# Performance work log

Hardware: AMD Instinct MI355X
Metric: run time of the kernel (lower is better)

The kernel has to match this reference:

```python
import jax, jax.numpy as jnp
import numpy as np

INIT_W = 0.1  # init_weight uniform range


def setup_inputs() -> dict:
    key = jax.random.key(0)
    kq, kk, kwq, kwk, ka = jax.random.split(key, 5)
    B, b, t_q, t_k = 2, 16, 64, 128
    qs = ks = nu = 512
    query = jax.random.normal(kq, (B, b, t_q, qs), dtype=jnp.float32)
    keys = jax.random.normal(kk, (B, b, t_k, ks), dtype=jnp.float32)
    # torch Linear weight layout: (out_features, in_features), per fusion slice
    Wq = (jax.random.uniform(kwq, (B, nu, qs), dtype=jnp.float32) * 2 - 1) * INIT_W
    Wk = (jax.random.uniform(kwk, (B, nu, ks), dtype=jnp.float32) * 2 - 1) * INIT_W
    linear_att = (jax.random.uniform(ka, (nu,), dtype=jnp.float32) * 2 - 1) * INIT_W
    return {"query": query, "keys": keys, "Wq": Wq, "Wk": Wk, "linear_att": linear_att}


def reference(query, keys, Wq, Wk, linear_att):
    # query: (B, b, t_q, query_size), keys: (B, b, t_k, key_size)
    # HFTA-fused linear projections (no bias): y = x @ W.T per fusion slice
    pq = jnp.einsum('Bbqi,Boi->Bbqo', query, Wq)   # (B, b, t_q, n)
    pk = jnp.einsum('Bbki,Boi->Bbko', keys, Wk)    # (B, b, t_k, n)
    # Bahdanau additive score: tanh(q + k) . v  (broadcast add over t_q x t_k)
    sum_qk = pq[:, :, :, None, :] + pk[:, :, None, :, :]   # (B, b, t_q, t_k, n)
    scores = jnp.einsum('Bbqkn,n->Bbqk', jnp.tanh(sum_qk), linear_att)
    scores_normalized = jax.nn.softmax(scores, axis=-1)    # (B, b, t_q, t_k)
    # context uses RAW keys (not projected)
    context = jnp.einsum('Bbqk,Bbkn->Bbqn', scores_normalized, keys)
    return context, scores_normalized
```

## Files before the change

### kernel.cpp

```cpp
#include <hip/hip_runtime.h>


#define DEV_INLINE __device__ __forceinline__

constexpr float C2    = 2.8853900817779268f;
constexpr float LOG2E = 1.4426950408889634f;

typedef _Float16 f16x8 __attribute__((ext_vector_type(8)));
typedef float    f32x16 __attribute__((ext_vector_type(16)));

DEV_INLINE unsigned int pk2(float a, float b) {
    auto h = __builtin_amdgcn_cvt_pkrtz(a, b);
    return __builtin_bit_cast(unsigned int, h);
}

DEV_INLINE float rcp_nr(float d) {
    float y = __builtin_bit_cast(float, 0x7EF311C3u - __builtin_bit_cast(unsigned int, d));
    y = y * (2.0f - d * y);
    y = y * (2.0f - d * y);
    return y;
}

#define GL2LDS16(g, l) __builtin_amdgcn_global_load_lds( \
    (const __attribute__((address_space(1))) void*)(g),  \
    (__attribute__((address_space(3))) void*)(l), 16, 0, 0)

__global__ __launch_bounds__(256)
void cvt_f16_kernel(const float* __restrict__ query, const float* __restrict__ keys,
                    const float* __restrict__ Wq,    const float* __restrict__ Wk,
                    uint2* __restrict__ dst)
{
    const int i4 = blockIdx.x * 256 + threadIdx.x;
    const float* src; int base;
    if (i4 < 262144)      { src = query; base = 0; }
    else if (i4 < 786432) { src = keys;  base = 262144; }
    else if (i4 < 917504) { src = Wq;    base = 786432; }
    else                  { src = Wk;    base = 917504; }
    const float4 v = *reinterpret_cast<const float4*>(src + (size_t)(i4 - base) * 4);
    dst[i4] = make_uint2(pk2(v.x, v.y), pk2(v.z, v.w));
}

__global__ __launch_bounds__(256)
void proj_mfma_kernel(const _Float16* __restrict__ X16,
                      float* __restrict__ pqT, float* __restrict__ pkT)
{
    __shared__ __align__(16) unsigned char smem[24576];

    const int bid = (blockIdx.x & 7) * 48 + (blockIdx.x >> 3);

    int Bi, mt, tt, tkshift;
    const _Float16 *Wb, *Xb; float* Y;
    if (bid < 128) {
        Bi = bid >> 6; mt = (bid >> 4) & 3; tt = bid & 15;
        Xb = X16 + ((size_t)Bi * 1024 + tt * 64) * 512;
        Wb = X16 + 3145728 + (size_t)Bi * 262144 + (size_t)(mt * 128) * 512;
        Y = pqT; tkshift = 6;
    } else {
        const int b2 = bid - 128;
        Bi = b2 >> 7; mt = (b2 >> 5) & 3; tt = b2 & 31;
        Xb = X16 + 1048576 + ((size_t)Bi * 2048 + tt * 64) * 512;
        Wb = X16 + 3670016 + (size_t)Bi * 262144 + (size_t)(mt * 128) * 512;
        Y = pkT; tkshift = 7;
    }
    const int tid = threadIdx.x;

    auto srcoff = [](int u) {
        const int row = u >> 2, s = (u & 3) ^ ((row >> 1) & 3);
        return (size_t)row * 512 + s * 8;
    };
    const _Float16* gA0 = Wb + srcoff(tid);
    const _Float16* gA1 = Wb + srcoff(tid + 256);
    const _Float16* gB  = Xb + srcoff(tid);
    unsigned char* const ldsA0 = smem + tid * 16;
    unsigned char* const ldsA1 = smem + 4096 + tid * 16;
    unsigned char* const ldsB  = smem + 8192 + tid * 16;

    const int wid = tid >> 6, lane = tid & 63;
    const int wm = wid >> 1, wn = wid & 1;
    const int r31 = lane & 31, h = lane >> 5;
    auto lofs = [](int row, int slot) {
        return row * 64 + ((slot ^ ((row >> 1) & 3)) * 16);
    };
    const int rowA0 = wm * 64 + r31, rowA1 = rowA0 + 32, rowB = wn * 32 + r31;
    const int a00 = lofs(rowA0, h),     a01 = lofs(rowA0, 2 + h);
    const int a10 = lofs(rowA1, h),     a11 = lofs(rowA1, 2 + h);
    const int b0  = 8192 + lofs(rowB, h), b1 = 8192 + lofs(rowB, 2 + h);

    f32x16 acc0, acc1;
#pragma unroll
    for (int i = 0; i < 16; ++i) { acc0[i] = 0.f; acc1[i] = 0.f; }

    GL2LDS16(gA0, ldsA0);
    GL2LDS16(gA1, ldsA1);
    GL2LDS16(gB,  ldsB);
    asm volatile("s_waitcnt vmcnt(0)" ::: "memory");
    __builtin_amdgcn_s_barrier();

    for (int ks = 0; ks < 16; ++ks) {
        const int buf = ks & 1;
        if (ks < 15) {
            const int ko = (ks + 1) * 32, bo = (buf ^ 1) * 12288;
            GL2LDS16(gA0 + ko, ldsA0 + bo);
            GL2LDS16(gA1 + ko, ldsA1 + bo);
            GL2LDS16(gB  + ko, ldsB  + bo);
        }
        const unsigned char* sb = smem + buf * 12288;
        const f16x8 fa00 = *reinterpret_cast<const f16x8*>(sb + a00);
        const f16x8 fa01 = *reinterpret_cast<const f16x8*>(sb + a01);
        const f16x8 fa10 = *reinterpret_cast<const f16x8*>(sb + a10);
        const f16x8 fa11 = *reinterpret_cast<const f16x8*>(sb + a11);
        const f16x8 fb0  = *reinterpret_cast<const f16x8*>(sb + b0);
        const f16x8 fb1  = *reinterpret_cast<const f16x8*>(sb + b1);
        acc0 = __builtin_amdgcn_mfma_f32_32x32x16_f16(fa00, fb0, acc0, 0, 0, 0);
        acc0 = __builtin_amdgcn_mfma_f32_32x32x16_f16(fa01, fb1, acc0, 0, 0, 0);
        acc1 = __builtin_amdgcn_mfma_f32_32x32x16_f16(fa10, fb0, acc1, 0, 0, 0);
        acc1 = __builtin_amdgcn_mfma_f32_32x32x16_f16(fa11, fb1, acc1, 0, 0, 0);
        if (ks < 15) {
            asm volatile("s_waitcnt vmcnt(0)" ::: "memory");
            __builtin_amdgcn_s_barrier();
        }
    }

    const int TK = 1 << tkshift;
    const int trow = tt * 64 + wn * 32 + r31;
    const int slice = Bi * 16 + (trow >> tkshift);
    const int t = trow & (TK - 1);
    const int nf0 = mt * 128 + wm * 64 + 4 * h;
#pragma unroll
    for (int ab = 0; ab < 2; ++ab) {
        const f32x16 acc = ab ? acc1 : acc0;
#pragma unroll
        for (int reg = 0; reg < 16; ++reg) {
            const int nf = nf0 + ab * 32 + (reg & 3) + 8 * (reg >> 2);
            Y[((size_t)(slice * 512 + nf) << tkshift) + t] = acc[reg] * C2;
        }
    }
}

DEV_INLINE float wave_rmax(float v) {
#pragma unroll
    for (int off = 32; off; off >>= 1) v = fmaxf(v, __shfl_xor(v, off, 64));
    return v;
}
DEV_INLINE float wave_rsum(float v) {
#pragma unroll
    for (int off = 32; off; off >>= 1) v += __shfl_xor(v, off, 64);
    return v;
}

__global__ __launch_bounds__(1024)
void score_ctx_kernel(const float* __restrict__ pqT,
                      const float* __restrict__ pkT,
                      const float* __restrict__ vatt,
                      const float* __restrict__ keys,
                      float* __restrict__ sc_out,
                      float* __restrict__ ctx)
{
    const int xcd = blockIdx.x & 7, ix = blockIdx.x >> 3;
    const int slice = xcd * 4 + (ix >> 4);
    const int q0    = (ix & 15) * 4;
    const int tid   = threadIdx.x;
    const int k     = tid & 127;
    const int nh    = tid >> 7;

    __shared__ __align__(16) float pql[512][4];
    __shared__ float wl[512];
    __shared__ float partial[7][4][128];
    __shared__ __align__(16) float sc[128][4];
    __shared__ __align__(16) float4 ctxp[4][4][128];
    __shared__ float wredm[8], wreds[8], wsum[8];

    if (tid < 512) {
        const float vv = vatt[tid];
        wl[tid] = -2.f * vv;
        const float4 q4 = *reinterpret_cast<const float4*>(
            pqT + ((size_t)slice * 512 + tid) * 64 + q0);
        *reinterpret_cast<float4*>(&pql[tid][0]) = q4;
        const float s = wave_rsum(vv);
        if ((tid & 63) == 0) wsum[tid >> 6] = s;
    }
    __syncthreads();
    float sumv = 0.f;
#pragma unroll
    for (int w = 0; w < 8; ++w) sumv += wsum[w];

    const float* __restrict__ pkp = pkT + ((size_t)slice * 512 + nh * 64) * 128 + k;
    float a0 = 0.f, a1 = 0.f, a2 = 0.f, a3 = 0.f;
#pragma unroll 4
    for (int n = 0; n < 64; ++n) {
        const float pk = pkp[(size_t)n * 128];
        const float4 pq4 = *reinterpret_cast<const float4*>(&pql[nh * 64 + n][0]);
        const float w = wl[nh * 64 + n];
        const float e0 = __builtin_amdgcn_exp2f(pq4.x + pk);
        const float e1 = __builtin_amdgcn_exp2f(pq4.y + pk);
        const float e2 = __builtin_amdgcn_exp2f(pq4.z + pk);
        const float e3 = __builtin_amdgcn_exp2f(pq4.w + pk);
        a0 = fmaf(w, rcp_nr(e0 + 1.f), a0);
        a1 = fmaf(w, rcp_nr(e1 + 1.f), a1);
        a2 = fmaf(w, rcp_nr(e2 + 1.f), a2);
        a3 = fmaf(w, rcp_nr(e3 + 1.f), a3);
    }
    if (nh) {
        partial[nh - 1][0][k] = a0; partial[nh - 1][1][k] = a1;
        partial[nh - 1][2][k] = a2; partial[nh - 1][3][k] = a3;
    }
    __syncthreads();
    if (!nh) {
        float s0 = a0 + sumv, s1 = a1 + sumv, s2 = a2 + sumv, s3 = a3 + sumv;
#pragma unroll
        for (int p = 0; p < 7; ++p) {
            s0 += partial[p][0][k]; s1 += partial[p][1][k];
            s2 += partial[p][2][k]; s3 += partial[p][3][k];
        }
        float4 sv; sv.x = s0; sv.y = s1; sv.z = s2; sv.w = s3;
        *reinterpret_cast<float4*>(&sc[k][0]) = sv;
    }
    __syncthreads();

    {
        const int j = nh & 3;
        float e = 0.f;
        if (tid < 512) {
            const float orig = sc[k][j];
            const float m0 = wave_rmax(orig);
            if ((tid & 63) == 0) wredm[tid >> 6] = m0;
            e = orig;
        }
        __syncthreads();
        if (tid < 512) {
            const float m = fmaxf(wredm[2 * j], wredm[2 * j + 1]);
            e = __builtin_amdgcn_exp2f((e - m) * LOG2E);
            const float ss = wave_rsum(e);
            if ((tid & 63) == 0) wreds[tid >> 6] = ss;
        }
        __syncthreads();
        if (tid < 512) {
            const float s = wreds[2 * j] + wreds[2 * j + 1];
            const float p = e * __builtin_amdgcn_rcpf(s);
            sc_out[((size_t)slice * 64 + q0 + j) * 128 + k] = p;
            sc[k][j] = p;
        }
    }
    __syncthreads();

    const int kg = nh, n4 = k;
    float4 acc0 = {0,0,0,0}, acc1 = {0,0,0,0}, acc2 = {0,0,0,0}, acc3 = {0,0,0,0};
    const float* __restrict__ kb = keys + (size_t)slice * 65536 + (size_t)(kg * 16) * 512 + n4 * 4;
#pragma unroll 4
    for (int r = 0; r < 16; ++r) {
        const float4 kv = *reinterpret_cast<const float4*>(kb + (size_t)r * 512);
        const float4 pv = *reinterpret_cast<const float4*>(&sc[kg * 16 + r][0]);
        acc0.x = fmaf(pv.x, kv.x, acc0.x); acc0.y = fmaf(pv.x, kv.y, acc0.y);
        acc0.z = fmaf(pv.x, kv.z, acc0.z); acc0.w = fmaf(pv.x, kv.w, acc0.w);
        acc1.x = fmaf(pv.y, kv.x, acc1.x); acc1.y = fmaf(pv.y, kv.y, acc1.y);
        acc1.z = fmaf(pv.y, kv.z, acc1.z); acc1.w = fmaf(pv.y, kv.w, acc1.w);
        acc2.x = fmaf(pv.z, kv.x, acc2.x); acc2.y = fmaf(pv.z, kv.y, acc2.y);
        acc2.z = fmaf(pv.z, kv.z, acc2.z); acc2.w = fmaf(pv.z, kv.w, acc2.w);
        acc3.x = fmaf(pv.w, kv.x, acc3.x); acc3.y = fmaf(pv.w, kv.y, acc3.y);
        acc3.z = fmaf(pv.w, kv.z, acc3.z); acc3.w = fmaf(pv.w, kv.w, acc3.w);
    }

    if (kg >= 4) {
        ctxp[kg - 4][0][n4] = acc0; ctxp[kg - 4][1][n4] = acc1;
        ctxp[kg - 4][2][n4] = acc2; ctxp[kg - 4][3][n4] = acc3;
    }
    __syncthreads();
    if (kg < 4) {
        const float4 o0 = ctxp[kg][0][n4], o1 = ctxp[kg][1][n4];
        const float4 o2 = ctxp[kg][2][n4], o3 = ctxp[kg][3][n4];
        acc0.x += o0.x; acc0.y += o0.y; acc0.z += o0.z; acc0.w += o0.w;
        acc1.x += o1.x; acc1.y += o1.y; acc1.z += o1.z; acc1.w += o1.w;
        acc2.x += o2.x; acc2.y += o2.y; acc2.z += o2.z; acc2.w += o2.w;
        acc3.x += o3.x; acc3.y += o3.y; acc3.z += o3.z; acc3.w += o3.w;
    }
    __syncthreads();
    if (kg == 2 || kg == 3) {
        ctxp[kg - 2][0][n4] = acc0; ctxp[kg - 2][1][n4] = acc1;
        ctxp[kg - 2][2][n4] = acc2; ctxp[kg - 2][3][n4] = acc3;
    }
    __syncthreads();
    if (kg < 2) {
        const float4 o0 = ctxp[kg][0][n4], o1 = ctxp[kg][1][n4];
        const float4 o2 = ctxp[kg][2][n4], o3 = ctxp[kg][3][n4];
        acc0.x += o0.x; acc0.y += o0.y; acc0.z += o0.z; acc0.w += o0.w;
        acc1.x += o1.x; acc1.y += o1.y; acc1.z += o1.z; acc1.w += o1.w;
        acc2.x += o2.x; acc2.y += o2.y; acc2.z += o2.z; acc2.w += o2.w;
        acc3.x += o3.x; acc3.y += o3.y; acc3.z += o3.z; acc3.w += o3.w;
    }
    __syncthreads();
    if (kg == 1) {
        ctxp[0][0][n4] = acc0; ctxp[0][1][n4] = acc1;
        ctxp[0][2][n4] = acc2; ctxp[0][3][n4] = acc3;
    }
    __syncthreads();
    if (kg == 0) {
        const float4 o0 = ctxp[0][0][n4], o1 = ctxp[0][1][n4];
        const float4 o2 = ctxp[0][2][n4], o3 = ctxp[0][3][n4];
        acc0.x += o0.x; acc0.y += o0.y; acc0.z += o0.z; acc0.w += o0.w;
        acc1.x += o1.x; acc1.y += o1.y; acc1.z += o1.z; acc1.w += o1.w;
        acc2.x += o2.x; acc2.y += o2.y; acc2.z += o2.z; acc2.w += o2.w;
        acc3.x += o3.x; acc3.y += o3.y; acc3.z += o3.z; acc3.w += o3.w;
        float* cb = ctx + ((size_t)slice * 64 + q0) * 512 + n4 * 4;
        *reinterpret_cast<float4*>(cb)             = acc0;
        *reinterpret_cast<float4*>(cb + 512)       = acc1;
        *reinterpret_cast<float4*>(cb + 2 * 512)   = acc2;
        *reinterpret_cast<float4*>(cb + 3 * 512)   = acc3;
    }
}

extern "C" void kernel_launch(void* const* d_in, const int* in_sizes, int n_in,
                              void* d_out, int out_size, void* d_ws, size_t ws_size,
                              hipStream_t stream)
{
    const float* query = (const float*)d_in[0];
    const float* keys  = (const float*)d_in[1];
    const float* Wq    = (const float*)d_in[2];
    const float* Wk    = (const float*)d_in[3];
    const float* vatt  = (const float*)d_in[4];

    float* ctx_out = (float*)d_out;
    float* sc_out  = ctx_out + (size_t)32 * 64 * 512;

    float* pqT = (float*)d_ws;
    float* pkT = pqT + (size_t)32 * 512 * 64;
    _Float16* X16 = (_Float16*)((char*)d_ws + 12 * 1024 * 1024);

    cvt_f16_kernel<<<dim3(4096), 256, 0, stream>>>(query, keys, Wq, Wk, (uint2*)X16);
    proj_mfma_kernel<<<dim3(384), 256, 0, stream>>>(X16, pqT, pkT);
    score_ctx_kernel<<<dim3(512), 1024, 0, stream>>>(pqT, pkT, vatt, keys, sc_out, ctx_out);
}
```

Baseline: 62.72 us.

## Precompute attention weight table upstream and read pq directly in score kernel

The -2*v weight table and the sum of v are now computed once, by an extra block appended to the conversion kernel, instead of in every score block. The score kernel drops the LDS staging of pq and the leading barrier, and reads pq and weights straight from global memory using wave-uniform addresses. Half the sigmoid reciprocals now use the hardware rcp instead of the Newton-refined one, which lowers accuracy slightly. The score buffer is also re-laid-out as [q][k], so the context loop can read probabilities with float4 loads.

```diff
diff --git a/kernel.cpp b/kernel.cpp
--- a/kernel.cpp
+++ b/kernel.cpp
@@ -25,11 +25,34 @@
     (const __attribute__((address_space(1))) void*)(g),  \
     (__attribute__((address_space(3))) void*)(l), 16, 0, 0)
 
+DEV_INLINE float wave_rsum(float v) {
+#pragma unroll
+    for (int off = 32; off; off >>= 1) v += __shfl_xor(v, off, 64);
+    return v;
+}
+DEV_INLINE float wave_rmax(float v) {
+#pragma unroll
+    for (int off = 32; off; off >>= 1) v = fmaxf(v, __shfl_xor(v, off, 64));
+    return v;
+}
+
 __global__ __launch_bounds__(256)
 void cvt_f16_kernel(const float* __restrict__ query, const float* __restrict__ keys,
                     const float* __restrict__ Wq,    const float* __restrict__ Wk,
-                    uint2* __restrict__ dst)
+                    const float* __restrict__ vatt,
+                    uint2* __restrict__ dst, float* __restrict__ wtab)
 {
+    if (blockIdx.x == 4096) {
+        __shared__ float ws4[4];
+        const int t = threadIdx.x;
+        const float v0 = vatt[t], v1 = vatt[t + 256];
+        wtab[t] = -2.f * v0; wtab[t + 256] = -2.f * v1;
+        const float s = wave_rsum(v0 + v1);
+        if ((t & 63) == 0) ws4[t >> 6] = s;
+        __syncthreads();
+        if (t == 0) wtab[512] = ws4[0] + ws4[1] + ws4[2] + ws4[3];
+        return;
+    }
     const int i4 = blockIdx.x * 256 + threadIdx.x;
     const float* src; int base;
     if (i4 < 262144)      { src = query; base = 0; }
@@ -137,21 +160,10 @@
     }
 }
 
-DEV_INLINE float wave_rmax(float v) {
-#pragma unroll
-    for (int off = 32; off; off >>= 1) v = fmaxf(v, __shfl_xor(v, off, 64));
-    return v;
-}
-DEV_INLINE float wave_rsum(float v) {
-#pragma unroll
-    for (int off = 32; off; off >>= 1) v += __shfl_xor(v, off, 64);
-    return v;
-}
-
 __global__ __launch_bounds__(1024)
 void score_ctx_kernel(const float* __restrict__ pqT,
                       const float* __restrict__ pkT,
-                      const float* __restrict__ vatt,
+                      const float* __restrict__ wtab,
                       const float* __restrict__ keys,
                       float* __restrict__ sc_out,
                       float* __restrict__ ctx)
@@ -163,42 +175,32 @@
     const int k     = tid & 127;
     const int nh    = tid >> 7;
 
-    __shared__ __align__(16) float pql[512][4];
-    __shared__ float wl[512];
     __shared__ float partial[7][4][128];
-    __shared__ __align__(16) float sc[128][4];
+    __shared__ __align__(16) float scQ[4][128];
     __shared__ __align__(16) float4 ctxp[4][4][128];
-    __shared__ float wredm[8], wreds[8], wsum[8];
-
-    if (tid < 512) {
-        const float vv = vatt[tid];
-        wl[tid] = -2.f * vv;
-        const float4 q4 = *reinterpret_cast<const float4*>(
-            pqT + ((size_t)slice * 512 + tid) * 64 + q0);
-        *reinterpret_cast<float4*>(&pql[tid][0]) = q4;
-        const float s = wave_rsum(vv);
-        if ((tid & 63) == 0) wsum[tid >> 6] = s;
-    }
-    __syncthreads();
-    float sumv = 0.f;
-#pragma unroll
-    for (int w = 0; w < 8; ++w) sumv += wsum[w];
-
-    const float* __restrict__ pkp = pkT + ((size_t)slice * 512 + nh * 64) * 128 + k;
+    __shared__ float wredm[8], wreds[8];
+
+    const float sumv = wtab[512];
+
+    const int wv = __builtin_amdgcn_readfirstlane(nh);
+    const float* __restrict__ pqb = pqT + ((size_t)slice * 512 + wv * 64) * 64 + q0;
+    const float* __restrict__ wb  = wtab + wv * 64;
+    const float* __restrict__ pkp = pkT + ((size_t)slice * 512 + wv * 64) * 128 + k;
+
     float a0 = 0.f, a1 = 0.f, a2 = 0.f, a3 = 0.f;
-#pragma unroll 4
+#pragma unroll 8
     for (int n = 0; n < 64; ++n) {
         const float pk = pkp[(size_t)n * 128];
-        const float4 pq4 = *reinterpret_cast<const float4*>(&pql[nh * 64 + n][0]);
-        const float w = wl[nh * 64 + n];
-        const float e0 = __builtin_amdgcn_exp2f(pq4.x + pk);
-        const float e1 = __builtin_amdgcn_exp2f(pq4.y + pk);
-        const float e2 = __builtin_amdgcn_exp2f(pq4.z + pk);
-        const float e3 = __builtin_amdgcn_exp2f(pq4.w + pk);
-        a0 = fmaf(w, rcp_nr(e0 + 1.f), a0);
-        a1 = fmaf(w, rcp_nr(e1 + 1.f), a1);
-        a2 = fmaf(w, rcp_nr(e2 + 1.f), a2);
-        a3 = fmaf(w, rcp_nr(e3 + 1.f), a3);
+        const float4 pq = *reinterpret_cast<const float4*>(pqb + n * 64);
+        const float w = wb[n];
+        const float e0 = __builtin_amdgcn_exp2f(pq.x + pk) + 1.f;
+        const float e1 = __builtin_amdgcn_exp2f(pq.y + pk) + 1.f;
+        const float e2 = __builtin_amdgcn_exp2f(pq.z + pk) + 1.f;
+        const float e3 = __builtin_amdgcn_exp2f(pq.w + pk) + 1.f;
+        a0 = fmaf(w, rcp_nr(e0), a0);
+        a1 = fmaf(w, rcp_nr(e1), a1);
+        a2 = fmaf(w, __builtin_amdgcn_rcpf(e2), a2);
+        a3 = fmaf(w, __builtin_amdgcn_rcpf(e3), a3);
     }
     if (nh) {
         partial[nh - 1][0][k] = a0; partial[nh - 1][1][k] = a1;
@@ -212,8 +214,7 @@
             s0 += partial[p][0][k]; s1 += partial[p][1][k];
             s2 += partial[p][2][k]; s3 += partial[p][3][k];
         }
-        float4 sv; sv.x = s0; sv.y = s1; sv.z = s2; sv.w = s3;
-        *reinterpret_cast<float4*>(&sc[k][0]) = sv;
+        scQ[0][k] = s0; scQ[1][k] = s1; scQ[2][k] = s2; scQ[3][k] = s3;
     }
     __syncthreads();
 
@@ -221,7 +222,7 @@
         const int j = nh & 3;
         float e = 0.f;
         if (tid < 512) {
-            const float orig = sc[k][j];
+            const float orig = scQ[j][k];
             const float m0 = wave_rmax(orig);
             if ((tid & 63) == 0) wredm[tid >> 6] = m0;
             e = orig;
@@ -238,7 +239,7 @@
             const float s = wreds[2 * j] + wreds[2 * j + 1];
             const float p = e * __builtin_amdgcn_rcpf(s);
             sc_out[((size_t)slice * 64 + q0 + j) * 128 + k] = p;
-            sc[k][j] = p;
+            scQ[j][k] = p;
         }
     }
     __syncthreads();
@@ -246,18 +247,28 @@
     const int kg = nh, n4 = k;
     float4 acc0 = {0,0,0,0}, acc1 = {0,0,0,0}, acc2 = {0,0,0,0}, acc3 = {0,0,0,0};
     const float* __restrict__ kb = keys + (size_t)slice * 65536 + (size_t)(kg * 16) * 512 + n4 * 4;
-#pragma unroll 4
-    for (int r = 0; r < 16; ++r) {
-        const float4 kv = *reinterpret_cast<const float4*>(kb + (size_t)r * 512);
-        const float4 pv = *reinterpret_cast<const float4*>(&sc[kg * 16 + r][0]);
-        acc0.x = fmaf(pv.x, kv.x, acc0.x); acc0.y = fmaf(pv.x, kv.y, acc0.y);
-        acc0.z = fmaf(pv.x, kv.z, acc0.z); acc0.w = fmaf(pv.x, kv.w, acc0.w);
-        acc1.x = fmaf(pv.y, kv.x, acc1.x); acc1.y = fmaf(pv.y, kv.y, acc1.y);
-        acc1.z = fmaf(pv.y, kv.z, acc1.z); acc1.w = fmaf(pv.y, kv.w, acc1.w);
-        acc2.x = fmaf(pv.z, kv.x, acc2.x); acc2.y = fmaf(pv.z, kv.y, acc2.y);
-        acc2.z = fmaf(pv.z, kv.z, acc2.z); acc2.w = fmaf(pv.z, kv.w, acc2.w);
-        acc3.x = fmaf(pv.w, kv.x, acc3.x); acc3.y = fmaf(pv.w, kv.y, acc3.y);
-        acc3.z = fmaf(pv.w, kv.z, acc3.z); acc3.w = fmaf(pv.w, kv.w, acc3.w);
+#pragma unroll
+    for (int r4 = 0; r4 < 4; ++r4) {
+        const float4 pv0 = *reinterpret_cast<const float4*>(&scQ[0][kg * 16 + r4 * 4]);
+        const float4 pv1 = *reinterpret_cast<const float4*>(&scQ[1][kg * 16 + r4 * 4]);
+        const float4 pv2 = *reinterpret_cast<const float4*>(&scQ[2][kg * 16 + r4 * 4]);
+        const float4 pv3 = *reinterpret_cast<const float4*>(&scQ[3][kg * 16 + r4 * 4]);
+        const float pa[4][4] = {{pv0.x, pv0.y, pv0.z, pv0.w},
+                                {pv1.x, pv1.y, pv1.z, pv1.w},
+                                {pv2.x, pv2.y, pv2.z, pv2.w},
+                                {pv3.x, pv3.y, pv3.z, pv3.w}};
+#pragma unroll
+        for (int rr = 0; rr < 4; ++rr) {
+            const float4 kv = *reinterpret_cast<const float4*>(kb + (size_t)(r4 * 4 + rr) * 512);
+            acc0.x = fmaf(pa[0][rr], kv.x, acc0.x); acc0.y = fmaf(pa[0][rr], kv.y, acc0.y);
+            acc0.z = fmaf(pa[0][rr], kv.z, acc0.z); acc0.w = fmaf(pa[0][rr], kv.w, acc0.w);
+            acc1.x = fmaf(pa[1][rr], kv.x, acc1.x); acc1.y = fmaf(pa[1][rr], kv.y, acc1.y);
+            acc1.z = fmaf(pa[1][rr], kv.z, acc1.z); acc1.w = fmaf(pa[1][rr], kv.w, acc1.w);
+            acc2.x = fmaf(pa[2][rr], kv.x, acc2.x); acc2.y = fmaf(pa[2][rr], kv.y, acc2.y);
+            acc2.z = fmaf(pa[2][rr], kv.z, acc2.z); acc2.w = fmaf(pa[2][rr], kv.w, acc2.w);
+            acc3.x = fmaf(pa[3][rr], kv.x, acc3.x); acc3.y = fmaf(pa[3][rr], kv.y, acc3.y);
+            acc3.z = fmaf(pa[3][rr], kv.z, acc3.z); acc3.w = fmaf(pa[3][rr], kv.w, acc3.w);
+        }
     }
 
     if (kg >= 4) {
@@ -324,8 +335,10 @@
     float* pqT = (float*)d_ws;
     float* pkT = pqT + (size_t)32 * 512 * 64;
     _Float16* X16 = (_Float16*)((char*)d_ws + 12 * 1024 * 1024);
-
-    cvt_f16_kernel<<<dim3(4096), 256, 0, stream>>>(query, keys, Wq, Wk, (uint2*)X16);
+    float* wtab = (float*)((char*)d_ws + 20 * 1024 * 1024);
+
+    cvt_f16_kernel<<<dim3(4097), 256, 0, stream>>>(query, keys, Wq, Wk, vatt,
+                                                   (uint2*)X16, wtab);
     proj_mfma_kernel<<<dim3(384), 256, 0, stream>>>(X16, pqT, pkT);
-    score_ctx_kernel<<<dim3(512), 1024, 0, stream>>>(pqT, pkT, vatt, keys, sc_out, ctx_out);
-}
+    score_ctx_kernel<<<dim3(512), 1024, 0, stream>>>(pqT, pkT, wtab, keys, sc_out, ctx_out);
+}
```

Result: faster. 54.08 us (-13.8%).
